# Optimization experiments

Measured on AMD Instinct MI355X. Metric: run time of the kernel, lower is better.

## Reference

```python
import jax, jax.numpy as jnp
import numpy as np

N_EMBED = 384

def setup_inputs() -> dict:
    key = jax.random.key(0)
    kx, kq, kk, kv = jax.random.split(key, 4)
    B, T, C = 512, 256, N_EMBED
    H = 64
    scale = 1.0 / np.sqrt(C)  # param init scale, keep activations sane
    x = jax.random.normal(kx, (B, T, C), dtype=jnp.float32)
    Wq = jax.random.normal(kq, (C, H), dtype=jnp.float32) * scale
    Wk = jax.random.normal(kk, (C, H), dtype=jnp.float32) * scale
    Wv = jax.random.normal(kv, (C, H), dtype=jnp.float32) * scale
    return {"x": x, "Wq": Wq, "Wk": Wk, "Wv": Wv}

def reference(x, Wq, Wk, Wv):
    B, T, C = x.shape
    q = jnp.einsum('btc,ch->bth', x, Wq)
    k = jnp.einsum('btc,ch->bth', x, Wk)
    v = jnp.einsum('btc,ch->bth', x, Wv)
    # NOTE: original scales by C**-0.5 with C = n_embed (384), not head_size.
    wei = jnp.einsum('bth,bsh->bts', q, k) * (C ** -0.5)  # [B,T,T]
    causal = jnp.tril(jnp.ones((T, T), dtype=bool))
    wei = jnp.where(causal, wei, -jnp.inf)
    wei = jax.nn.softmax(wei, axis=-1)
    out = jnp.einsum('bts,bsh->bth', wei, v)  # [B,T,H]
    return out
```

## Files before the change

### kernel.cpp

```cpp
#include <hip/hip_runtime.h>
#include <hip/hip_bf16.h>


constexpr int BSZ  = 512;
constexpr int TT   = 256;
constexpr int CDIM = 384;
constexpr int HDIM = 64;
constexpr int NQKV = 192;
constexpr float SCALE = 0.051031036307982884f;
constexpr int BTST = 392;

typedef __attribute__((ext_vector_type(8))) short bf16x8;
typedef __attribute__((ext_vector_type(4))) float f32x4;

__device__ inline unsigned short f2bf(float f) {
    __hip_bfloat16 h = __float2bfloat16(f);
    return *(unsigned short*)&h;
}
__device__ inline bf16x8 pack8(float4 a, float4 b) {
    unsigned short p[8] = { f2bf(a.x), f2bf(a.y), f2bf(a.z), f2bf(a.w),
                            f2bf(b.x), f2bf(b.y), f2bf(b.z), f2bf(b.w) };
    return *(bf16x8*)p;
}

__global__ __launch_bounds__(256) void prep_bt(
    const float* __restrict__ Wq, const float* __restrict__ Wk,
    const float* __restrict__ Wv, unsigned short* __restrict__ bt)
{
    int idx = blockIdx.x * 256 + threadIdx.x;
    if (idx >= NQKV * CDIM) return;
    int n = idx / CDIM, k = idx - n * CDIM;
    const float* W = (n < 64) ? Wq : (n < 128) ? Wk : Wv;
    bt[idx] = f2bf(W[(size_t)k * HDIM + (n & 63)]);
}

__global__ __launch_bounds__(1024) void fused(
    const float* __restrict__ x, const unsigned short* __restrict__ bt,
    float* __restrict__ out)
{
    __shared__ __align__(16) unsigned short smem[NQKV * BTST];
    unsigned short* btl = smem;
    unsigned short* qs  = smem;
    unsigned short* kl  = smem + 16384;
    unsigned short* vt  = smem + 32768;

    const int b = blockIdx.x, tid = threadIdx.x;
    const int w = tid >> 6, lane = tid & 63;
    const int lr = lane & 15, lk = lane >> 4;

    const float* xr0 = x + ((size_t)b * TT + 16 * w + lr) * CDIM + lk * 8;

    float4 pA[2], pB[2], pC[2];
#define LDCH(P, ks) { \
    P[0] = *(const float4*)&xr0[(ks) * 32];     \
    P[1] = *(const float4*)&xr0[(ks) * 32 + 4]; }
#define STEP(P, ks, cond) { \
    bf16x8 a = pack8(P[0], P[1]); \
    if (cond) LDCH(P, (ks) + 3); \
    _Pragma("unroll") \
    for (int ni = 0; ni < 12; ++ni) { \
        bf16x8 bb = *(const bf16x8*)&btl[(ni * 16 + lr) * BTST + (ks) * 32 + lk * 8]; \
        acc[ni] = __builtin_amdgcn_mfma_f32_16x16x32_bf16(a, bb, acc[ni], 0, 0, 0); \
    } }

    LDCH(pA, 0) LDCH(pB, 1) LDCH(pC, 2)

    #pragma unroll
    for (int p = 0; p < 9; ++p) {
        int i = p * 1024 + tid;
        int row = i / 48, c8 = i - row * 48;
        *(uint4*)&btl[row * BTST + c8 * 8] = ((const uint4*)bt)[i];
    }
    __syncthreads();

    f32x4 acc[12];
    #pragma unroll
    for (int ni = 0; ni < 12; ++ni) acc[ni] = (f32x4){0.f, 0.f, 0.f, 0.f};

    #pragma unroll
    for (int kk = 0; kk < 4; ++kk) {
        STEP(pA, 3 * kk + 0, kk < 3)
        STEP(pB, 3 * kk + 1, kk < 3)
        STEP(pC, 3 * kk + 2, kk < 3)
    }
#undef LDCH
#undef STEP
    __syncthreads();

    unsigned short* pq = qs + w * 1024;
    #pragma unroll
    for (int ni = 0; ni < 4; ++ni)
        #pragma unroll
        for (int r = 0; r < 4; ++r) {
            int qr = lk * 4 + r;
            int h  = ni * 16 + lr;
            pq[qr * 64 + (h ^ ((qr & 7) << 3))] = f2bf(acc[ni][r] * SCALE);
        }
    #pragma unroll
    for (int ni = 4; ni < 8; ++ni)
        #pragma unroll
        for (int r = 0; r < 4; ++r) {
            int row = 16 * w + lk * 4 + r;
            int c2  = (ni - 4) * 16 + lr;
            kl[row * 64 + (c2 ^ ((row & 7) << 3))] = f2bf(acc[ni][r]);
        }
    #pragma unroll
    for (int ni = 8; ni < 12; ++ni) {
        int h  = (ni - 8) * 16 + lr;
        int t0 = 16 * w + lk * 4;
        unsigned short pk[4];
        #pragma unroll
        for (int r = 0; r < 4; ++r) pk[r] = f2bf(acc[ni][r]);
        *(uint2*)&vt[h * 256 + (t0 ^ ((h & 7) << 3))] = *(uint2*)pk;
    }
    __syncthreads();

    const int q0 = 16 * w;
    bf16x8 qa[2];
    #pragma unroll
    for (int kc = 0; kc < 2; ++kc)
        qa[kc] = *(const bf16x8*)&pq[lr * 64 + ((kc * 32 + lk * 8) ^ ((lr & 7) << 3))];

    f32x4 oacc[4];
    float mrow[4], lpart[4];
    #pragma unroll
    for (int nh = 0; nh < 4; ++nh) oacc[nh] = (f32x4){0.f, 0.f, 0.f, 0.f};
    #pragma unroll
    for (int r = 0; r < 4; ++r) { mrow[r] = -INFINITY; lpart[r] = 0.f; }

    const int lastt = w >> 2;
    for (int st = 0; st <= lastt; ++st) {
        f32x4 sa[4];
        #pragma unroll
        for (int ni = 0; ni < 4; ++ni) sa[ni] = (f32x4){0.f, 0.f, 0.f, 0.f};
        #pragma unroll
        for (int ni = 0; ni < 4; ++ni) {
            int row = st * 64 + ni * 16 + lr;
            #pragma unroll
            for (int kc = 0; kc < 2; ++kc) {
                bf16x8 kb = *(const bf16x8*)
                    &kl[row * 64 + ((kc * 32 + lk * 8) ^ ((lr & 7) << 3))];
                sa[ni] = __builtin_amdgcn_mfma_f32_16x16x32_bf16(qa[kc], kb, sa[ni], 0, 0, 0);
            }
        }
        if (st == lastt) {
            #pragma unroll
            for (int ni = 0; ni < 4; ++ni) {
                int sg = st * 64 + ni * 16 + lr;
                #pragma unroll
                for (int r = 0; r < 4; ++r) {
                    int qg = q0 + lk * 4 + r;
                    if (sg > qg) sa[ni][r] = -INFINITY;
                }
            }
        }
        float pm[4];
        #pragma unroll
        for (int r = 0; r < 4; ++r)
            pm[r] = fmaxf(fmaxf(sa[0][r], sa[1][r]), fmaxf(sa[2][r], sa[3][r]));
        #pragma unroll
        for (int stp = 1; stp < 16; stp <<= 1)
            #pragma unroll
            for (int r = 0; r < 4; ++r)
                pm[r] = fmaxf(pm[r], __shfl_xor(pm[r], stp));
        float mnew[4];
        #pragma unroll
        for (int r = 0; r < 4; ++r) {
            float mn = fmaxf(mrow[r], pm[r]);
            float corr = __expf(mrow[r] - mn);
            mrow[r] = mn; mnew[r] = mn;
            lpart[r] *= corr;
            #pragma unroll
            for (int nh = 0; nh < 4; ++nh) oacc[nh][r] *= corr;
        }
        #pragma unroll
        for (int ni = 0; ni < 4; ++ni) {
            int s = ni * 16 + lr;
            #pragma unroll
            for (int r = 0; r < 4; ++r) {
                float p = __expf(sa[ni][r] - mnew[r]);
                lpart[r] += p;
                int qr = lk * 4 + r;
                pq[qr * 64 + (s ^ ((qr & 7) << 3))] = f2bf(p);
            }
        }
        bf16x8 pa[2];
        #pragma unroll
        for (int kc = 0; kc < 2; ++kc)
            pa[kc] = *(const bf16x8*)
                &pq[lr * 64 + ((kc * 32 + lk * 8) ^ ((lr & 7) << 3))];
        #pragma unroll
        for (int nh = 0; nh < 4; ++nh) {
            int hrow = nh * 16 + lr;
            #pragma unroll
            for (int kc = 0; kc < 2; ++kc) {
                bf16x8 vb = *(const bf16x8*)
                    &vt[hrow * 256 + ((st * 64 + kc * 32 + lk * 8) ^ ((hrow & 7) << 3))];
                oacc[nh] = __builtin_amdgcn_mfma_f32_16x16x32_bf16(pa[kc], vb, oacc[nh], 0, 0, 0);
            }
        }
    }

    float linv[4];
    #pragma unroll
    for (int r = 0; r < 4; ++r) {
        float l = lpart[r];
        #pragma unroll
        for (int stp = 1; stp < 16; stp <<= 1) l += __shfl_xor(l, stp);
        linv[r] = 1.0f / l;
    }
    #pragma unroll
    for (int nh = 0; nh < 4; ++nh)
        #pragma unroll
        for (int r = 0; r < 4; ++r) {
            size_t row = (size_t)b * TT + q0 + lk * 4 + r;
            out[row * HDIM + nh * 16 + lr] = oacc[nh][r] * linv[r];
        }
}

extern "C" void kernel_launch(void* const* d_in, const int* in_sizes, int n_in,
                              void* d_out, int out_size, void* d_ws, size_t ws_size,
                              hipStream_t stream)
{
    const float* x  = (const float*)d_in[0];
    const float* Wq = (const float*)d_in[1];
    const float* Wk = (const float*)d_in[2];
    const float* Wv = (const float*)d_in[3];
    unsigned short* bt = (unsigned short*)d_ws;
    float* out = (float*)d_out;

    prep_bt<<<(NQKV * CDIM + 255) / 256, 256, 0, stream>>>(Wq, Wk, Wv, bt);
    fused<<<BSZ, 1024, 0, stream>>>(x, bt, out);
}
```

Before: 65.50 us.

## Compute transposed S tile and build P operand in registers via permlane swaps

Swaps the MFMA operand order so each lane holds a query row's scores along the key axis. The row max and sum now need only two cross-lane shuffles instead of a four-step reduction. The P matrix for the PV MFMA is built in registers with packed bf16 conversion and permlane16/32 swaps instead of a round-trip through shared memory. The running max is then broadcast back to the output layout for rescaling. This adds extra shuffles and inline asm that depends on gfx950 instructions.

Result: faster. 61.41 us, median of 3 (-6.2%).

```diff
diff --git a/kernel.cpp b/kernel.cpp
--- a/kernel.cpp
+++ b/kernel.cpp
@@ -22,6 +22,13 @@
                             f2bf(b.x), f2bf(b.y), f2bf(b.z), f2bf(b.w) };
     return *(bf16x8*)p;
 }
+__device__ inline unsigned cvtpk(float lo, float hi) {
+    unsigned r;
+    asm volatile("v_cvt_pk_bf16_f32 %0, %1, %2" : "=v"(r) : "v"(lo), "v"(hi));
+    return r;
+}
+#define PLSWAP32(a, b) asm volatile("v_permlane32_swap_b32 %0, %1" : "+v"(a), "+v"(b))
+#define PLSWAP16(a, b) asm volatile("v_permlane16_swap_b32 %0, %1" : "+v"(a), "+v"(b))
 
 __global__ __launch_bounds__(256) void prep_bt(
     const float* __restrict__ Wq, const float* __restrict__ Wk,
@@ -122,11 +129,13 @@
         qa[kc] = *(const bf16x8*)&pq[lr * 64 + ((kc * 32 + lk * 8) ^ ((lr & 7) << 3))];
 
     f32x4 oacc[4];
-    float mrow[4], lpart[4];
+    float mrowL = -INFINITY;
+    float lpart = 0.f;
+    float mrowT[4];
     #pragma unroll
     for (int nh = 0; nh < 4; ++nh) oacc[nh] = (f32x4){0.f, 0.f, 0.f, 0.f};
     #pragma unroll
-    for (int r = 0; r < 4; ++r) { mrow[r] = -INFINITY; lpart[r] = 0.f; }
+    for (int r = 0; r < 4; ++r) mrowT[r] = -INFINITY;
 
     const int lastt = w >> 2;
     for (int st = 0; st <= lastt; ++st) {
@@ -139,56 +148,63 @@
             #pragma unroll
             for (int kc = 0; kc < 2; ++kc) {
                 bf16x8 kb = *(const bf16x8*)
-                    &kl[row * 64 + ((kc * 32 + lk * 8) ^ ((lr & 7) << 3))];
-                sa[ni] = __builtin_amdgcn_mfma_f32_16x16x32_bf16(qa[kc], kb, sa[ni], 0, 0, 0);
+                    &kl[row * 64 + ((kc * 32 + lk * 8) ^ ((row & 7) << 3))];
+                sa[ni] = __builtin_amdgcn_mfma_f32_16x16x32_bf16(kb, qa[kc], sa[ni], 0, 0, 0);
             }
         }
         if (st == lastt) {
             #pragma unroll
             for (int ni = 0; ni < 4; ++ni) {
-                int sg = st * 64 + ni * 16 + lr;
                 #pragma unroll
                 for (int r = 0; r < 4; ++r) {
-                    int qg = q0 + lk * 4 + r;
-                    if (sg > qg) sa[ni][r] = -INFINITY;
+                    int sg = st * 64 + ni * 16 + lk * 4 + r;
+                    if (sg > q0 + lr) sa[ni][r] = -INFINITY;
                 }
             }
         }
-        float pm[4];
-        #pragma unroll
-        for (int r = 0; r < 4; ++r)
-            pm[r] = fmaxf(fmaxf(sa[0][r], sa[1][r]), fmaxf(sa[2][r], sa[3][r]));
-        #pragma unroll
-        for (int stp = 1; stp < 16; stp <<= 1)
-            #pragma unroll
-            for (int r = 0; r < 4; ++r)
-                pm[r] = fmaxf(pm[r], __shfl_xor(pm[r], stp));
-        float mnew[4];
-        #pragma unroll
-        for (int r = 0; r < 4; ++r) {
-            float mn = fmaxf(mrow[r], pm[r]);
-            float corr = __expf(mrow[r] - mn);
-            mrow[r] = mn; mnew[r] = mn;
-            lpart[r] *= corr;
-            #pragma unroll
-            for (int nh = 0; nh < 4; ++nh) oacc[nh][r] *= corr;
-        }
+        float pm = sa[0][0];
+        #pragma unroll
+        for (int ni = 0; ni < 4; ++ni)
+            #pragma unroll
+            for (int r = 0; r < 4; ++r) pm = fmaxf(pm, sa[ni][r]);
+        pm = fmaxf(pm, __shfl_xor(pm, 16));
+        pm = fmaxf(pm, __shfl_xor(pm, 32));
+        float mn = fmaxf(mrowL, pm);
+        float corr = __expf(mrowL - mn);
+        mrowL = mn;
+        lpart *= corr;
+        #pragma unroll
+        for (int ni = 0; ni < 4; ++ni)
+            #pragma unroll
+            for (int r = 0; r < 4; ++r) {
+                float p = __expf(sa[ni][r] - mn);
+                sa[ni][r] = p;
+                lpart += p;
+            }
+        #pragma unroll
+        for (int r = 0; r < 4; ++r) {
+            float mt = __shfl(mn, lk * 4 + r);
+            float ct = __expf(mrowT[r] - mt);
+            mrowT[r] = mt;
+            #pragma unroll
+            for (int nh = 0; nh < 4; ++nh) oacc[nh][r] *= ct;
+        }
+        unsigned Wp[4][2];
         #pragma unroll
         for (int ni = 0; ni < 4; ++ni) {
-            int s = ni * 16 + lr;
-            #pragma unroll
-            for (int r = 0; r < 4; ++r) {
-                float p = __expf(sa[ni][r] - mnew[r]);
-                lpart[r] += p;
-                int qr = lk * 4 + r;
-                pq[qr * 64 + (s ^ ((qr & 7) << 3))] = f2bf(p);
-            }
+            Wp[ni][0] = cvtpk(sa[ni][0], sa[ni][1]);
+            Wp[ni][1] = cvtpk(sa[ni][2], sa[ni][3]);
         }
         bf16x8 pa[2];
         #pragma unroll
-        for (int kc = 0; kc < 2; ++kc)
-            pa[kc] = *(const bf16x8*)
-                &pq[lr * 64 + ((kc * 32 + lk * 8) ^ ((lr & 7) << 3))];
+        for (int kc = 0; kc < 2; ++kc) {
+            unsigned x0 = Wp[2 * kc][0], y0 = Wp[2 * kc + 1][0];
+            PLSWAP32(x0, y0); PLSWAP16(x0, y0);
+            unsigned x1 = Wp[2 * kc][1], y1 = Wp[2 * kc + 1][1];
+            PLSWAP32(x1, y1); PLSWAP16(x1, y1);
+            unsigned wq[4] = {x0, x1, y0, y1};
+            pa[kc] = *(bf16x8*)wq;
+        }
         #pragma unroll
         for (int nh = 0; nh < 4; ++nh) {
             int hrow = nh * 16 + lr;
@@ -201,14 +217,13 @@
         }
     }
 
+    float lsum = lpart;
+    lsum += __shfl_xor(lsum, 16);
+    lsum += __shfl_xor(lsum, 32);
     float linv[4];
     #pragma unroll
-    for (int r = 0; r < 4; ++r) {
-        float l = lpart[r];
-        #pragma unroll
-        for (int stp = 1; stp < 16; stp <<= 1) l += __shfl_xor(l, stp);
-        linv[r] = 1.0f / l;
-    }
+    for (int r = 0; r < 4; ++r)
+        linv[r] = 1.0f / __shfl(lsum, lk * 4 + r);
     #pragma unroll
     for (int nh = 0; nh < 4; ++nh)
         #pragma unroll
```
